# Kernel optimization log

Measured on AMD Instinct MI355X. Metric: run time of the kernel, lower is better.

Reference implementation:

```python
import jax, jax.numpy as jnp
import numpy as np

B, T, C = 2, 2048, 768
NH = 12
HS = C // NH


def setup_inputs() -> dict:
    key = jax.random.key(0)
    k1, k2, k3 = jax.random.split(key, 3)
    x = jax.random.normal(k1, (B, T, C), dtype=jnp.float32)
    # c_attn: Linear(C, 3C). Stored as (C, 3C) so y = x @ w + b (same math as torch x @ W.T + b).
    w_attn = jax.random.normal(k2, (C, 3 * C), dtype=jnp.float32) * (1.0 / np.sqrt(C))
    b_attn = jax.random.normal(k3, (3 * C,), dtype=jnp.float32) * 0.02
    return {"x": x, "w_attn": w_attn, "b_attn": b_attn}


def reference(x, w_attn, b_attn):
    b, t, c = x.shape
    qkv = x @ w_attn + b_attn                      # [B, T, 3C]
    q, k, v = jnp.split(qkv, 3, axis=-1)
    # [B, T, C] -> [B, NH, T, HS]
    q = q.reshape(b, t, NH, HS).transpose(0, 2, 1, 3)
    k = k.reshape(b, t, NH, HS).transpose(0, 2, 1, 3)
    v = v.reshape(b, t, NH, HS).transpose(0, 2, 1, 3)
    scale = 1.0 / np.sqrt(HS).astype(np.float32)
    wei = jnp.einsum("bhqd,bhkd->bhqk", q, k) * scale   # [B, NH, T, T]
    causal = jnp.tril(jnp.ones((t, t), dtype=bool))
    wei = jnp.where(causal[None, None, :, :], wei, -jnp.inf)
    wei = jax.nn.softmax(wei, axis=-1)
    out = jnp.einsum("bhqk,bhkd->bhqd", wei, v)          # [B, NH, T, HS]
    # NOTE: original module returns here, before head-merge / output projection.
    return out
```

## Files before the change

kernel.cpp:

```cpp
#include <hip/hip_runtime.h>

typedef __bf16 bf16_t;
typedef __bf16 bf16x8 __attribute__((ext_vector_type(8)));
typedef __bf16 bf16x4 __attribute__((ext_vector_type(4)));
typedef _Float16 f16x4 __attribute__((ext_vector_type(4)));
typedef _Float16 f16x8 __attribute__((ext_vector_type(8)));
typedef float f32x4 __attribute__((ext_vector_type(4)));

#define B_   2
#define T_   2048
#define C_   768
#define NH_  12
#define HS_  64
#define N3_  2304
#define M_   4096
#define NOUT 3145728
#define NQ   49152

__device__ __forceinline__ bf16_t f2bf(float f) {
  unsigned u = __builtin_bit_cast(unsigned, f);
  u += 0x7fffu + ((u >> 16) & 1u);
  unsigned short s = (unsigned short)(u >> 16);
  return __builtin_bit_cast(bf16_t, s);
}

__global__ __launch_bounds__(256) void cvt_xw_kernel(const float* __restrict__ x,
                                                     const float* __restrict__ w,
                                                     bf16_t* __restrict__ xb,
                                                     bf16_t* __restrict__ wt) {
  __shared__ float tile[32][33];
  int bx = blockIdx.x;
  if (bx < 3072) {
    int i = (bx * 256 + threadIdx.x) * 4;
    float4 v = *reinterpret_cast<const float4*>(x + i);
    xb[i + 0] = f2bf(v.x);
    xb[i + 1] = f2bf(v.y);
    xb[i + 2] = f2bf(v.z);
    xb[i + 3] = f2bf(v.w);
  } else {
    int b = bx - 3072;
    int k0 = (b % 24) * 32, n0 = (b / 24) * 32;
    int tx = threadIdx.x & 31, ty = threadIdx.x >> 5;
#pragma unroll
    for (int i = 0; i < 4; i++)
      tile[ty + i * 8][tx] = w[(size_t)(k0 + ty + i * 8) * N3_ + n0 + tx];
    __syncthreads();
#pragma unroll
    for (int i = 0; i < 4; i++)
      wt[(size_t)(n0 + ty + i * 8) * C_ + k0 + tx] = f2bf(tile[tx][ty + i * 8]);
  }
}

__global__ __launch_bounds__(256) void gemm_qkv(const bf16_t* __restrict__ xb,
                                                const bf16_t* __restrict__ wt,
                                                const float* __restrict__ bias,
                                                bf16_t* __restrict__ qout,
                                                bf16_t* __restrict__ kout,
                                                _Float16* __restrict__ va) {
  __shared__ bf16_t As[128 * 32];
  __shared__ bf16_t Bs[128 * 32];
  const int tid = threadIdx.x;
  const int lane = tid & 63, wave = tid >> 6;
  const int wm = wave >> 1, wn = wave & 1;
  const int quad = lane >> 4, l15 = lane & 15;
  const int row0 = blockIdx.y * 128;
  const int col0 = blockIdx.x * 128;
  const bool isqk = (col0 < 1536);

  f32x4 acc[4][4];
#pragma unroll
  for (int mi = 0; mi < 4; mi++)
#pragma unroll
    for (int ni = 0; ni < 4; ni++) acc[mi][ni] = f32x4{0.f, 0.f, 0.f, 0.f};

  for (int k0 = 0; k0 < C_; k0 += 32) {
#pragma unroll
    for (int c = 0; c < 2; c++) {
      int chunk = c * 256 + tid;
      int r = chunk >> 2, qd = chunk & 3;
      const bf16_t* ga = xb + (size_t)(row0 + r) * C_ + k0 + qd * 8;
      const bf16_t* gb = wt + (size_t)(col0 + r) * C_ + k0 + qd * 8;
      char* la = (char*)As + (size_t)(c * 256 + wave * 64) * 16;
      char* lb = (char*)Bs + (size_t)(c * 256 + wave * 64) * 16;
      __builtin_amdgcn_global_load_lds((const __attribute__((address_space(1))) void*)ga,
                                       (__attribute__((address_space(3))) void*)la, 16, 0, 0);
      __builtin_amdgcn_global_load_lds((const __attribute__((address_space(1))) void*)gb,
                                       (__attribute__((address_space(3))) void*)lb, 16, 0, 0);
    }
    __syncthreads();

    bf16x8 af[4], bfr[4];
#pragma unroll
    for (int mi = 0; mi < 4; mi++)
      af[mi] = *reinterpret_cast<const bf16x8*>(&As[(wm * 64 + mi * 16 + l15) * 32 + quad * 8]);
#pragma unroll
    for (int ni = 0; ni < 4; ni++)
      bfr[ni] = *reinterpret_cast<const bf16x8*>(&Bs[(wn * 64 + ni * 16 + l15) * 32 + quad * 8]);
    if (isqk) {
#pragma unroll
      for (int mi = 0; mi < 4; mi++)
#pragma unroll
        for (int ni = 0; ni < 4; ni++)
          acc[mi][ni] = __builtin_amdgcn_mfma_f32_16x16x32_bf16(bfr[ni], af[mi], acc[mi][ni], 0, 0, 0);
    } else {
#pragma unroll
      for (int mi = 0; mi < 4; mi++)
#pragma unroll
        for (int ni = 0; ni < 4; ni++)
          acc[mi][ni] = __builtin_amdgcn_mfma_f32_16x16x32_bf16(af[mi], bfr[ni], acc[mi][ni], 0, 0, 0);
    }
    __syncthreads();
  }

  if (isqk) {
#pragma unroll
    for (int mi = 0; mi < 4; mi++) {
      int t = row0 + wm * 64 + mi * 16 + l15;
      int b = t >> 11, tt = t & 2047;
#pragma unroll
      for (int ni = 0; ni < 4; ni++) {
        int cN0 = col0 + wn * 64 + ni * 16 + quad * 4;
        int which = cN0 / 768;
        int rem = cN0 - which * 768;
        int h = rem >> 6, d0 = rem & 63;
        float4 bv = *reinterpret_cast<const float4*>(bias + cN0);
        bf16x4 pack;
        pack[0] = f2bf(acc[mi][ni][0] + bv.x);
        pack[1] = f2bf(acc[mi][ni][1] + bv.y);
        pack[2] = f2bf(acc[mi][ni][2] + bv.z);
        pack[3] = f2bf(acc[mi][ni][3] + bv.w);
        bf16_t* dst = which ? kout : qout;
        *reinterpret_cast<bf16x4*>(dst + (((size_t)b * NH_ + h) * T_ + tt) * HS_ + d0) = pack;
      }
    }
  } else {
#pragma unroll
    for (int mi = 0; mi < 4; mi++) {
      int trow = row0 + wm * 64 + mi * 16 + quad * 4;
      int b = trow >> 11, tt = trow & 2047;
      int kt = tt >> 6, nj = (tt >> 4) & 3, qd = (tt >> 2) & 3;
#pragma unroll
      for (int ni = 0; ni < 4; ni++) {
        int cN = col0 + wn * 64 + ni * 16 + l15;
        int rem = cN - 1536;
        int h = rem >> 6, d = rem & 63;
        int bh = b * NH_ + h;
        float bv = bias[cN];
        f16x4 pk;
#pragma unroll
        for (int r = 0; r < 4; r++) pk[r] = (_Float16)(acc[mi][ni][r] + bv);
        size_t off = ((((((size_t)bh * 32 + kt) * 4 + nj) * 4 + qd) * 16 + (d & 15)) * 16) + (d >> 4) * 4;
        *reinterpret_cast<f16x4*>(va + off) = pk;
      }
    }
  }
}

__global__ __launch_bounds__(256) void attn_kernel(const bf16_t* __restrict__ qb,
                                                   const bf16_t* __restrict__ kb,
                                                   const _Float16* __restrict__ va,
                                                   float* __restrict__ opart,
                                                   float* __restrict__ lpart) {
  __shared__ bf16_t Ks[2][64][72];
  __shared__ _Float16 Vs[2][4][2][64][8];
  const int tid = threadIdx.x;
  const int lane = tid & 63, wave = tid >> 6;
  const int quad = lane >> 4, l15 = lane & 15;
  const int pairIdx = (int)blockIdx.x >> 1;
  const int half = (int)blockIdx.x & 1;
  const int bh = (int)blockIdx.z * NH_ + (int)blockIdx.y;
  const bf16_t* Qg = qb + (size_t)bh * T_ * HS_;
  const bf16_t* Kg = kb + (size_t)bh * T_ * HS_;
  const _Float16* Vg = va + (size_t)bh * 32 * 4096;

  const int krow = tid >> 2, kcol = (tid & 3) * 16;
  const int vni = tid >> 6, vlane = tid & 63;

  int4 rk0, rk1, rv0, rv1;
  auto GLOAD = [&](int kt) {
    const char* kp = (const char*)(Kg + (size_t)kt * 64 * HS_) + krow * 128 + kcol * 2;
    rk0 = *reinterpret_cast<const int4*>(kp);
    rk1 = *reinterpret_cast<const int4*>(kp + 16);
    const char* vp = (const char*)(Vg + (size_t)kt * 4096) + tid * 32;
    rv0 = *reinterpret_cast<const int4*>(vp);
    rv1 = *reinterpret_cast<const int4*>(vp + 16);
  };
  auto SSTORE = [&](int buf) {
    char* kd = (char*)&Ks[buf][krow][kcol];
    *reinterpret_cast<int4*>(kd) = rk0;
    *reinterpret_cast<int4*>(kd + 16) = rk1;
    *reinterpret_cast<int4*>(&Vs[buf][vni][0][vlane][0]) = rv0;
    *reinterpret_cast<int4*>(&Vs[buf][vni][1][vlane][0]) = rv1;
  };

#pragma unroll
  for (int part = 0; part < 2; part++) {
    const int qtile = part ? pairIdx : 31 - pairIdx;
    const int qrow_base = qtile * 64 + wave * 16;
    const int qmax = qrow_base + 15;
    const int qcol = qrow_base + l15;
    const int nkt = qtile + 1;
    const int khalf = (nkt + 1) >> 1;
    const int kt0 = half ? khalf : 0;
    const int kt1 = half ? nkt : khalf;

    bf16x8 bq0 = *reinterpret_cast<const bf16x8*>(Qg + (size_t)qcol * HS_ + quad * 8);
    bf16x8 bq1 = *reinterpret_cast<const bf16x8*>(Qg + (size_t)qcol * HS_ + 32 + quad * 8);

    float lsum = 0.f;
    f32x4 Oacc[4];
#pragma unroll
    for (int mi = 0; mi < 4; mi++) Oacc[mi] = f32x4{0.f, 0.f, 0.f, 0.f};

    if (kt1 > kt0) {
      GLOAD(kt0);
      __syncthreads();
      SSTORE(0);
      __syncthreads();

      for (int kt = kt0; kt < kt1; kt++) {
        const int cur = (kt - kt0) & 1;
        const bool last = (kt + 1 >= kt1);
        if (!last) GLOAD(kt + 1);

        const bool diag = (kt == nkt - 1);
        f16x4 pf[4];
#pragma unroll
        for (int ni = 0; ni < 4; ni++) {
          if (diag && (kt * 64 + ni * 16 > qmax)) continue;
          bf16x8 ka0 = *reinterpret_cast<const bf16x8*>(&Ks[cur][ni * 16 + l15][quad * 8]);
          bf16x8 ka1 = *reinterpret_cast<const bf16x8*>(&Ks[cur][ni * 16 + l15][32 + quad * 8]);
          f32x4 s = {0.f, 0.f, 0.f, 0.f};
          s = __builtin_amdgcn_mfma_f32_16x16x32_bf16(ka0, bq0, s, 0, 0, 0);
          s = __builtin_amdgcn_mfma_f32_16x16x32_bf16(ka1, bq1, s, 0, 0, 0);
#pragma unroll
          for (int r = 0; r < 4; r++) {
            float p = __builtin_amdgcn_exp2f(s[r] * 0.18033688011112042f);
            if (diag) {
              int j = kt * 64 + ni * 16 + quad * 4 + r;
              if (j > qcol) p = 0.f;
            }
            lsum += p;
            pf[ni][r] = (_Float16)p;
          }
        }
#pragma unroll
        for (int ni = 0; ni < 4; ni++) {
          if (diag && (kt * 64 + ni * 16 > qmax)) continue;
#pragma unroll
          for (int p = 0; p < 2; p++) {
            f16x8 vv = *reinterpret_cast<const f16x8*>(&Vs[cur][ni][p][lane][0]);
            f16x4 lo = __builtin_shufflevector(vv, vv, 0, 1, 2, 3);
            f16x4 hi = __builtin_shufflevector(vv, vv, 4, 5, 6, 7);
            Oacc[2 * p]     = __builtin_amdgcn_mfma_f32_16x16x16f16(lo, pf[ni], Oacc[2 * p], 0, 0, 0);
            Oacc[2 * p + 1] = __builtin_amdgcn_mfma_f32_16x16x16f16(hi, pf[ni], Oacc[2 * p + 1], 0, 0, 0);
          }
        }

        if (!last) {
          SSTORE(1 - cur);
          __syncthreads();
        }
      }
    }

    lsum += __shfl_xor(lsum, 16, 64);
    lsum += __shfl_xor(lsum, 32, 64);

    float* Op = opart + (size_t)half * NOUT + ((size_t)bh * T_ + qcol) * HS_;
#pragma unroll
    for (int mi = 0; mi < 4; mi++)
      *reinterpret_cast<f32x4*>(Op + mi * 16 + quad * 4) = Oacc[mi];
    if (lane < 16)
      lpart[(size_t)half * NQ + (size_t)bh * T_ + qrow_base + l15] = lsum;
  }
}

__global__ __launch_bounds__(256) void attn_combine(const float* __restrict__ opart,
                                                    const float* __restrict__ lpart,
                                                    float* __restrict__ out) {
  const int idx = blockIdx.x * 256 + threadIdx.x;
  const int base = idx * 4;
  const int q = idx >> 4;
  f32x4 a = *reinterpret_cast<const f32x4*>(opart + base);
  f32x4 b = *reinterpret_cast<const f32x4*>(opart + NOUT + base);
  float rinv = 1.0f / (lpart[q] + lpart[NQ + q]);
  f32x4 o = (a + b) * rinv;
  *reinterpret_cast<f32x4*>(out + base) = o;
}

extern "C" void kernel_launch(void* const* d_in, const int* in_sizes, int n_in,
                              void* d_out, int out_size, void* d_ws, size_t ws_size,
                              hipStream_t stream) {
  const float* x = (const float*)d_in[0];
  const float* w = (const float*)d_in[1];
  const float* bias = (const float*)d_in[2];
  float* out = (float*)d_out;

  char* ws = (char*)d_ws;
  bf16_t* xb = (bf16_t*)(ws);
  bf16_t* wt = (bf16_t*)(ws + 6291456);
  bf16_t* qb = (bf16_t*)(ws + 6291456 + 3538944);
  bf16_t* kb = qb + 3145728;
  _Float16* va = (_Float16*)(kb + 3145728);
  float* opart = (float*)((char*)va + 6291456);
  float* lpart = opart + 2 * NOUT;

  cvt_xw_kernel<<<dim3(3072 + 1728), dim3(256), 0, stream>>>(x, w, xb, wt);
  gemm_qkv<<<dim3(N3_ / 128, M_ / 128), dim3(256), 0, stream>>>(xb, wt, bias, qb, kb, va);
  attn_kernel<<<dim3(32, NH_, B_), dim3(256), 0, stream>>>(qb, kb, va, opart, lpart);
  attn_combine<<<dim3(NOUT / 1024), dim3(256), 0, stream>>>(opart, lpart, out);
}
```

Baseline: 157.3 us.

## Process 128 query rows per block and read V fragments directly from global

Each wave now handles two 16-row query groups, so every K tile staged in LDS is reused across 128 query rows instead of 64. The grid shrinks to 16 paired blocks per head, with the key range split at tile j+1 between the two halves. V is no longer staged in shared memory; each lane loads its pre-swizzled fp16 fragments straight from global, which removes the V LDS traffic but exposes global latency inside the loop. Launch bounds now request two blocks per SM, and the doubled accumulators raise register pressure.

Measured after the change: 174.4 us. +10.9%, slower.

```diff
diff --git a/kernel.cpp b/kernel.cpp
--- a/kernel.cpp
+++ b/kernel.cpp
@@ -156,17 +156,16 @@
   }
 }
 
-__global__ __launch_bounds__(256) void attn_kernel(const bf16_t* __restrict__ qb,
-                                                   const bf16_t* __restrict__ kb,
-                                                   const _Float16* __restrict__ va,
-                                                   float* __restrict__ opart,
-                                                   float* __restrict__ lpart) {
+__global__ __launch_bounds__(256, 2) void attn_kernel(const bf16_t* __restrict__ qb,
+                                                      const bf16_t* __restrict__ kb,
+                                                      const _Float16* __restrict__ va,
+                                                      float* __restrict__ opart,
+                                                      float* __restrict__ lpart) {
   __shared__ bf16_t Ks[2][64][72];
-  __shared__ _Float16 Vs[2][4][2][64][8];
   const int tid = threadIdx.x;
   const int lane = tid & 63, wave = tid >> 6;
   const int quad = lane >> 4, l15 = lane & 15;
-  const int pairIdx = (int)blockIdx.x >> 1;
+  const int pr = (int)blockIdx.x >> 1;
   const int half = (int)blockIdx.x & 1;
   const int bh = (int)blockIdx.z * NH_ + (int)blockIdx.y;
   const bf16_t* Qg = qb + (size_t)bh * T_ * HS_;
@@ -174,105 +173,137 @@
   const _Float16* Vg = va + (size_t)bh * 32 * 4096;
 
   const int krow = tid >> 2, kcol = (tid & 3) * 16;
-  const int vni = tid >> 6, vlane = tid & 63;
-
-  int4 rk0, rk1, rv0, rv1;
+  int4 rk0, rk1;
   auto GLOAD = [&](int kt) {
     const char* kp = (const char*)(Kg + (size_t)kt * 64 * HS_) + krow * 128 + kcol * 2;
     rk0 = *reinterpret_cast<const int4*>(kp);
     rk1 = *reinterpret_cast<const int4*>(kp + 16);
-    const char* vp = (const char*)(Vg + (size_t)kt * 4096) + tid * 32;
-    rv0 = *reinterpret_cast<const int4*>(vp);
-    rv1 = *reinterpret_cast<const int4*>(vp + 16);
   };
   auto SSTORE = [&](int buf) {
     char* kd = (char*)&Ks[buf][krow][kcol];
     *reinterpret_cast<int4*>(kd) = rk0;
     *reinterpret_cast<int4*>(kd + 16) = rk1;
-    *reinterpret_cast<int4*>(&Vs[buf][vni][0][vlane][0]) = rv0;
-    *reinterpret_cast<int4*>(&Vs[buf][vni][1][vlane][0]) = rv1;
   };
 
 #pragma unroll
   for (int part = 0; part < 2; part++) {
-    const int qtile = part ? pairIdx : 31 - pairIdx;
-    const int qrow_base = qtile * 64 + wave * 16;
-    const int qmax = qrow_base + 15;
-    const int qcol = qrow_base + l15;
-    const int nkt = qtile + 1;
-    const int khalf = (nkt + 1) >> 1;
-    const int kt0 = half ? khalf : 0;
-    const int kt1 = half ? nkt : khalf;
-
-    bf16x8 bq0 = *reinterpret_cast<const bf16x8*>(Qg + (size_t)qcol * HS_ + quad * 8);
-    bf16x8 bq1 = *reinterpret_cast<const bf16x8*>(Qg + (size_t)qcol * HS_ + 32 + quad * 8);
-
-    float lsum = 0.f;
-    f32x4 Oacc[4];
-#pragma unroll
-    for (int mi = 0; mi < 4; mi++) Oacc[mi] = f32x4{0.f, 0.f, 0.f, 0.f};
-
-    if (kt1 > kt0) {
-      GLOAD(kt0);
-      __syncthreads();
-      SSTORE(0);
-      __syncthreads();
-
-      for (int kt = kt0; kt < kt1; kt++) {
-        const int cur = (kt - kt0) & 1;
-        const bool last = (kt + 1 >= kt1);
-        if (!last) GLOAD(kt + 1);
-
-        const bool diag = (kt == nkt - 1);
-        f16x4 pf[4];
-#pragma unroll
-        for (int ni = 0; ni < 4; ni++) {
-          if (diag && (kt * 64 + ni * 16 > qmax)) continue;
-          bf16x8 ka0 = *reinterpret_cast<const bf16x8*>(&Ks[cur][ni * 16 + l15][quad * 8]);
-          bf16x8 ka1 = *reinterpret_cast<const bf16x8*>(&Ks[cur][ni * 16 + l15][32 + quad * 8]);
+    const int j = part ? pr : 15 - pr;
+    const int qb0 = j * 128;
+    const int g0 = qb0 + wave * 16;
+    const int g1 = qb0 + 64 + wave * 16;
+    const int q0 = g0 + l15, q1 = g1 + l15;
+    const int nkt = 2 * j + 2;
+    const int kt0 = half ? (j + 1) : 0;
+    const int kt1 = half ? nkt : (j + 1);
+    const int dt0 = g0 >> 6;
+    const int dt1 = g1 >> 6;
+
+    bf16x8 bq00 = *reinterpret_cast<const bf16x8*>(Qg + (size_t)q0 * HS_ + quad * 8);
+    bf16x8 bq01 = *reinterpret_cast<const bf16x8*>(Qg + (size_t)q0 * HS_ + 32 + quad * 8);
+    bf16x8 bq10 = *reinterpret_cast<const bf16x8*>(Qg + (size_t)q1 * HS_ + quad * 8);
+    bf16x8 bq11 = *reinterpret_cast<const bf16x8*>(Qg + (size_t)q1 * HS_ + 32 + quad * 8);
+
+    float ls0 = 0.f, ls1 = 0.f;
+    f32x4 O0[4], O1[4];
+#pragma unroll
+    for (int mi = 0; mi < 4; mi++) { O0[mi] = f32x4{0.f, 0.f, 0.f, 0.f}; O1[mi] = f32x4{0.f, 0.f, 0.f, 0.f}; }
+
+    GLOAD(kt0);
+    __syncthreads();
+    SSTORE(0);
+    __syncthreads();
+
+    for (int kt = kt0; kt < kt1; kt++) {
+      const int cur = (kt - kt0) & 1;
+      const bool last = (kt + 1 >= kt1);
+      if (!last) GLOAD(kt + 1);
+
+      f16x8 vl[4][2];
+      const _Float16* Vt = Vg + (size_t)kt * 4096;
+#pragma unroll
+      for (int ni = 0; ni < 4; ni++)
+#pragma unroll
+        for (int p2 = 0; p2 < 2; p2++)
+          vl[ni][p2] = *reinterpret_cast<const f16x8*>(Vt + ni * 1024 + lane * 16 + p2 * 8);
+
+      const bool act0 = (kt <= dt0);
+      const bool dg0 = (kt == dt0);
+      const bool dg1 = (kt == dt1);
+      f16x4 pf0[4], pf1[4];
+#pragma unroll
+      for (int ni = 0; ni < 4; ni++) {
+        const int jbase = kt * 64 + ni * 16;
+        const bool s0 = act0 && !(dg0 && jbase > g0 + 15);
+        const bool s1 = !(dg1 && jbase > g1 + 15);
+        if (!s0 && !s1) continue;
+        bf16x8 ka0 = *reinterpret_cast<const bf16x8*>(&Ks[cur][ni * 16 + l15][quad * 8]);
+        bf16x8 ka1 = *reinterpret_cast<const bf16x8*>(&Ks[cur][ni * 16 + l15][32 + quad * 8]);
+        if (s0) {
           f32x4 s = {0.f, 0.f, 0.f, 0.f};
-          s = __builtin_amdgcn_mfma_f32_16x16x32_bf16(ka0, bq0, s, 0, 0, 0);
-          s = __builtin_amdgcn_mfma_f32_16x16x32_bf16(ka1, bq1, s, 0, 0, 0);
+          s = __builtin_amdgcn_mfma_f32_16x16x32_bf16(ka0, bq00, s, 0, 0, 0);
+          s = __builtin_amdgcn_mfma_f32_16x16x32_bf16(ka1, bq01, s, 0, 0, 0);
 #pragma unroll
           for (int r = 0; r < 4; r++) {
             float p = __builtin_amdgcn_exp2f(s[r] * 0.18033688011112042f);
-            if (diag) {
-              int j = kt * 64 + ni * 16 + quad * 4 + r;
-              if (j > qcol) p = 0.f;
-            }
-            lsum += p;
-            pf[ni][r] = (_Float16)p;
+            if (dg0 && (jbase + quad * 4 + r > q0)) p = 0.f;
+            ls0 += p;
+            pf0[ni][r] = (_Float16)p;
           }
         }
-#pragma unroll
-        for (int ni = 0; ni < 4; ni++) {
-          if (diag && (kt * 64 + ni * 16 > qmax)) continue;
-#pragma unroll
-          for (int p = 0; p < 2; p++) {
-            f16x8 vv = *reinterpret_cast<const f16x8*>(&Vs[cur][ni][p][lane][0]);
-            f16x4 lo = __builtin_shufflevector(vv, vv, 0, 1, 2, 3);
-            f16x4 hi = __builtin_shufflevector(vv, vv, 4, 5, 6, 7);
-            Oacc[2 * p]     = __builtin_amdgcn_mfma_f32_16x16x16f16(lo, pf[ni], Oacc[2 * p], 0, 0, 0);
-            Oacc[2 * p + 1] = __builtin_amdgcn_mfma_f32_16x16x16f16(hi, pf[ni], Oacc[2 * p + 1], 0, 0, 0);
+        if (s1) {
+          f32x4 s = {0.f, 0.f, 0.f, 0.f};
+          s = __builtin_amdgcn_mfma_f32_16x16x32_bf16(ka0, bq10, s, 0, 0, 0);
+          s = __builtin_amdgcn_mfma_f32_16x16x32_bf16(ka1, bq11, s, 0, 0, 0);
+#pragma unroll
+          for (int r = 0; r < 4; r++) {
+            float p = __builtin_amdgcn_exp2f(s[r] * 0.18033688011112042f);
+            if (dg1 && (jbase + quad * 4 + r > q1)) p = 0.f;
+            ls1 += p;
+            pf1[ni][r] = (_Float16)p;
           }
         }
-
-        if (!last) {
-          SSTORE(1 - cur);
-          __syncthreads();
+      }
+#pragma unroll
+      for (int ni = 0; ni < 4; ni++) {
+        const int jbase = kt * 64 + ni * 16;
+        const bool s0 = act0 && !(dg0 && jbase > g0 + 15);
+        const bool s1 = !(dg1 && jbase > g1 + 15);
+        if (!s0 && !s1) continue;
+#pragma unroll
+        for (int p2 = 0; p2 < 2; p2++) {
+          f16x4 lo = __builtin_shufflevector(vl[ni][p2], vl[ni][p2], 0, 1, 2, 3);
+          f16x4 hi = __builtin_shufflevector(vl[ni][p2], vl[ni][p2], 4, 5, 6, 7);
+          if (s0) {
+            O0[2 * p2]     = __builtin_amdgcn_mfma_f32_16x16x16f16(lo, pf0[ni], O0[2 * p2], 0, 0, 0);
+            O0[2 * p2 + 1] = __builtin_amdgcn_mfma_f32_16x16x16f16(hi, pf0[ni], O0[2 * p2 + 1], 0, 0, 0);
+          }
+          if (s1) {
+            O1[2 * p2]     = __builtin_amdgcn_mfma_f32_16x16x16f16(lo, pf1[ni], O1[2 * p2], 0, 0, 0);
+            O1[2 * p2 + 1] = __builtin_amdgcn_mfma_f32_16x16x16f16(hi, pf1[ni], O1[2 * p2 + 1], 0, 0, 0);
+          }
         }
       }
-    }
-
-    lsum += __shfl_xor(lsum, 16, 64);
-    lsum += __shfl_xor(lsum, 32, 64);
-
-    float* Op = opart + (size_t)half * NOUT + ((size_t)bh * T_ + qcol) * HS_;
-#pragma unroll
-    for (int mi = 0; mi < 4; mi++)
-      *reinterpret_cast<f32x4*>(Op + mi * 16 + quad * 4) = Oacc[mi];
-    if (lane < 16)
-      lpart[(size_t)half * NQ + (size_t)bh * T_ + qrow_base + l15] = lsum;
+
+      if (!last) {
+        SSTORE(1 - cur);
+        __syncthreads();
+      }
+    }
+
+    ls0 += __shfl_xor(ls0, 16, 64); ls0 += __shfl_xor(ls0, 32, 64);
+    ls1 += __shfl_xor(ls1, 16, 64); ls1 += __shfl_xor(ls1, 32, 64);
+
+    float* Op0 = opart + (size_t)half * NOUT + ((size_t)bh * T_ + q0) * HS_;
+    float* Op1 = opart + (size_t)half * NOUT + ((size_t)bh * T_ + q1) * HS_;
+#pragma unroll
+    for (int mi = 0; mi < 4; mi++) {
+      *reinterpret_cast<f32x4*>(Op0 + mi * 16 + quad * 4) = O0[mi];
+      *reinterpret_cast<f32x4*>(Op1 + mi * 16 + quad * 4) = O1[mi];
+    }
+    if (lane < 16) {
+      lpart[(size_t)half * NQ + (size_t)bh * T_ + g0 + l15] = ls0;
+      lpart[(size_t)half * NQ + (size_t)bh * T_ + g1 + l15] = ls1;
+    }
   }
 }
 
@@ -308,6 +339,6 @@
 
   cvt_xw_kernel<<<dim3(3072 + 1728), dim3(256), 0, stream>>>(x, w, xb, wt);
   gemm_qkv<<<dim3(N3_ / 128, M_ / 128), dim3(256), 0, stream>>>(xb, wt, bias, qb, kb, va);
-  attn_kernel<<<dim3(32, NH_, B_), dim3(256), 0, stream>>>(qb, kb, va, opart, lpart);
+  attn_kernel<<<dim3(16, NH_, B_), dim3(256), 0, stream>>>(qb, kb, va, opart, lpart);
   attn_combine<<<dim3(NOUT / 1024), dim3(256), 0, stream>>>(opart, lpart, out);
 }
```
